# Optimization experiments

Measured on AMD Instinct MI355X. Metric: run time of the kernel, lower is better.

The kernel has to match this reference:

```python
import jax, jax.numpy as jnp
import numpy as np

IRR_IN = 4
IRR_OUT = 4
N_SCALAR = 64
E = 1_000_000
DIM = IRR_IN * IRR_OUT * 2  # 32
HID = 2 * DIM               # 64

# ir_1: swap-pair gather index [1,0,3,2,5,4,7,6]
IR_1 = np.concatenate([np.array([1, 0]) + 2 * i for i in range(IRR_IN)])
# ir_2: alternating sign [1,-1,1,-1,...]
IR_2 = np.ones(2 * IRR_IN, dtype=np.float32)
IR_2[1::2] = -1.0


def setup_inputs() -> dict:
    key = jax.random.key(0)
    ks = jax.random.split(key, 4)
    x = jax.random.normal(ks[0], (E, IRR_IN, 2), dtype=jnp.float32)
    s = jax.random.normal(ks[1], (E, N_SCALAR), dtype=jnp.float32)
    W1 = jax.random.normal(ks[2], (N_SCALAR, HID), dtype=jnp.float32) * (1.0 / np.sqrt(N_SCALAR))
    b1 = jnp.zeros((HID,), dtype=jnp.float32)
    W2 = jax.random.normal(ks[3], (HID, DIM), dtype=jnp.float32) * (1.0 / np.sqrt(HID))
    b2 = jnp.zeros((DIM,), dtype=jnp.float32)
    return {"x": x, "s": s, "W1": W1, "b1": b1, "W2": W2, "b2": b2}


def reference(x, s, W1, b1, W2, b2):
    ir1 = jnp.asarray(IR_1)
    ir2 = jnp.asarray(IR_2)
    # per-edge MLP producing raw weights: [E, irr_out, 2*irr_in]
    h = jax.nn.relu(s @ W1 + b1)
    w = (h @ W2 + b2).reshape(-1, IRR_OUT, 2 * IRR_IN)
    w_1 = w[:, :, ir1]        # pair-swapped copy
    w_2 = w * ir2             # sign-alternated copy
    # stack -> [E, 2, irr_out, 2*irr_in]; permute -> [E, 2*irr_in, irr_out, 2]
    wm = jnp.stack((w_2, w_1), axis=1).transpose(0, 3, 2, 1)
    wm = wm.reshape(-1, 2 * IRR_IN, 2 * IRR_OUT)  # [E, 2*irr_in, 2*irr_out]
    xf = x.reshape(-1, 2 * IRR_IN)                # [E, 2*irr_in]
    out = jnp.einsum('ei,eio->eo', xf, wm)        # tiny per-edge matvec
    return out.reshape(-1, IRR_OUT, 2)
```

## Files before the change

### kernel.cpp

```cpp
#include <hip/hip_runtime.h>
#include <hip/hip_bf16.h>

typedef __bf16 bf16x8 __attribute__((ext_vector_type(8)));
typedef float  f32x4  __attribute__((ext_vector_type(4)));

__global__ __launch_bounds__(256) void so2_fused_kernel(
    const float* __restrict__ x, const float* __restrict__ s,
    const float* __restrict__ W1, const float* __restrict__ b1v,
    const float* __restrict__ W2, const float* __restrict__ b2v,
    float* __restrict__ out, int E)
{
  __shared__ unsigned short lds_w1t[64 * 64];
  __shared__ unsigned short lds_w2t[32 * 64];
  __shared__ float lds_b1[64];
  __shared__ float lds_b2[32];
  __shared__ char lds_hw[4][8192];

  const int tid  = threadIdx.x;
  const int wid  = tid >> 6;
  const int lane = tid & 63;
  const int lrow = lane & 15;
  const int lg   = lane >> 4;

  const int web = blockIdx.x * 256 + wid * 64;
  const bool wave_active = (web < E);

  f32x4 sv[4][4];
  {
    const int base_e = wave_active ? web : 0;
    #pragma unroll
    for (int mt = 0; mt < 4; ++mt) {
      int er = base_e + mt * 16 + lrow;
      er = er < E ? er : E - 1;
      const float* sp = s + (size_t)er * 64 + lg * 8;
      sv[mt][0] = *(const f32x4*)(sp);
      sv[mt][1] = *(const f32x4*)(sp + 4);
      sv[mt][2] = *(const f32x4*)(sp + 32);
      sv[mt][3] = *(const f32x4*)(sp + 36);
    }
  }

  #pragma unroll
  for (int it = 0; it < 16; ++it) {
    int i = it * 256 + tid;
    int k = i >> 6, j = i & 63;
    int byte = (j << 7) + (k << 1);
    byte ^= (j & 7) << 4;
    *(unsigned short*)((char*)lds_w1t + byte) =
        __builtin_bit_cast(unsigned short, (__bf16)W1[i]);
  }
  #pragma unroll
  for (int it = 0; it < 8; ++it) {
    int i = it * 256 + tid;
    int k = i >> 5, d = i & 31;
    int byte = (d << 7) + (k << 1);
    byte ^= (d & 7) << 4;
    *(unsigned short*)((char*)lds_w2t + byte) =
        __builtin_bit_cast(unsigned short, (__bf16)W2[i]);
  }
  if (tid < 64) lds_b1[tid] = b1v[tid];
  if (tid >= 64 && tid < 96) lds_b2[tid - 64] = b2v[tid - 64];
  __syncthreads();
  if (!wave_active) return;

  char* hbuf = lds_hw[wid];

  bf16x8 af[4][2];
  #pragma unroll
  for (int mt = 0; mt < 4; ++mt) {
    #pragma unroll
    for (int h = 0; h < 2; ++h) {
      #pragma unroll
      for (int i = 0; i < 4; ++i) {
        af[mt][h][i]     = (__bf16)sv[mt][h * 2][i];
        af[mt][h][i + 4] = (__bf16)sv[mt][h * 2 + 1][i];
      }
    }
  }

  #pragma unroll
  for (int nt = 0; nt < 4; ++nt) {
    const int j = nt * 16 + lrow;
    bf16x8 bfr[2];
    #pragma unroll
    for (int h = 0; h < 2; ++h) {
      int byte = (j << 7) + ((h * 32 + lg * 8) << 1);
      byte ^= (j & 7) << 4;
      bfr[h] = *(const bf16x8*)((const char*)lds_w1t + byte);
    }
    const float bj = lds_b1[j];
    #pragma unroll
    for (int mt = 0; mt < 4; ++mt) {
      f32x4 acc = {0.f, 0.f, 0.f, 0.f};
      acc = __builtin_amdgcn_mfma_f32_16x16x32_bf16(af[mt][0], bfr[0], acc, 0, 0, 0);
      acc = __builtin_amdgcn_mfma_f32_16x16x32_bf16(af[mt][1], bfr[1], acc, 0, 0, 0);
      #pragma unroll
      for (int r = 0; r < 4; ++r) {
        float hv = fmaxf(acc[r] + bj, 0.f);
        int row = mt * 16 + lg * 4 + r;
        int byte = (row << 7) + (j << 1);
        byte ^= (row & 7) << 4;
        *(unsigned short*)(hbuf + byte) =
            __builtin_bit_cast(unsigned short, (__bf16)hv);
      }
    }
  }

  bf16x8 a2[4][2];
  #pragma unroll
  for (int mt = 0; mt < 4; ++mt) {
    #pragma unroll
    for (int h = 0; h < 2; ++h) {
      int row = mt * 16 + lrow;
      int byte = (row << 7) + ((h * 32 + lg * 8) << 1);
      byte ^= (row & 7) << 4;
      a2[mt][h] = *(const bf16x8*)(hbuf + byte);
    }
  }
  bf16x8 b2f[2][2];
  #pragma unroll
  for (int nt = 0; nt < 2; ++nt) {
    #pragma unroll
    for (int h = 0; h < 2; ++h) {
      int d = nt * 16 + lrow;
      int byte = (d << 7) + ((h * 32 + lg * 8) << 1);
      byte ^= (d & 7) << 4;
      b2f[nt][h] = *(const bf16x8*)((const char*)lds_w2t + byte);
    }
  }
  f32x4 wacc[4][2];
  #pragma unroll
  for (int mt = 0; mt < 4; ++mt) {
    #pragma unroll
    for (int nt = 0; nt < 2; ++nt) {
      f32x4 acc = {0.f, 0.f, 0.f, 0.f};
      acc = __builtin_amdgcn_mfma_f32_16x16x32_bf16(a2[mt][0], b2f[nt][0], acc, 0, 0, 0);
      acc = __builtin_amdgcn_mfma_f32_16x16x32_bf16(a2[mt][1], b2f[nt][1], acc, 0, 0, 0);
      wacc[mt][nt] = acc;
    }
  }

  #pragma unroll
  for (int nt = 0; nt < 2; ++nt) {
    const int d = nt * 16 + lrow;
    const float bd = lds_b2[d];
    #pragma unroll
    for (int mt = 0; mt < 4; ++mt) {
      f32x4 wout;
      #pragma unroll
      for (int r = 0; r < 4; ++r) wout[r] = wacc[mt][nt][r] + bd;
      int byte = (d << 8) + ((mt * 16 + lg * 4) << 2);
      byte ^= (d & 7) << 4;
      *(f32x4*)(hbuf + byte) = wout;
    }
  }

  const int e = web + lane;
  const float* xp = x + (size_t)(e < E ? e : E - 1) * 8;
  f32x4 x0 = *(const f32x4*)xp;
  f32x4 x1 = *(const f32x4*)(xp + 4);

  float wv32[32];
  #pragma unroll
  for (int d = 0; d < 32; ++d) {
    int byte = (d << 8) + (lane << 2);
    byte ^= (d & 7) << 4;
    wv32[d] = *(const float*)(hbuf + byte);
  }

  f32x4 o0, o1;
  #pragma unroll
  for (int o = 0; o < 4; ++o) {
    float orv = 0.f, oiv = 0.f;
    #pragma unroll
    for (int p = 0; p < 4; ++p) {
      float xr = (p < 2) ? x0[2 * p]     : x1[2 * p - 4];
      float xi = (p < 2) ? x0[2 * p + 1] : x1[2 * p - 3];
      float wr = wv32[o * 8 + 2 * p];
      float wi = wv32[o * 8 + 2 * p + 1];
      orv = fmaf(xr, wr, orv);
      orv = fmaf(-xi, wi, orv);
      oiv = fmaf(xr, wi, oiv);
      oiv = fmaf(xi, wr, oiv);
    }
    if (o < 2) { o0[2 * o] = orv; o0[2 * o + 1] = oiv; }
    else       { o1[2 * o - 4] = orv; o1[2 * o - 3] = oiv; }
  }
  if (e < E) {
    float* op = out + (size_t)e * 8;
    *(f32x4*)op       = o0;
    *(f32x4*)(op + 4) = o1;
  }
}

extern "C" void kernel_launch(void* const* d_in, const int* in_sizes, int n_in,
                              void* d_out, int out_size, void* d_ws, size_t ws_size,
                              hipStream_t stream) {
  const float* x  = (const float*)d_in[0];
  const float* s  = (const float*)d_in[1];
  const float* W1 = (const float*)d_in[2];
  const float* b1 = (const float*)d_in[3];
  const float* W2 = (const float*)d_in[4];
  const float* b2 = (const float*)d_in[5];
  float* out = (float*)d_out;
  const int E = in_sizes[0] / 8;
  const int blocks = (E + 255) / 256;
  so2_fused_kernel<<<blocks, 256, 0, stream>>>(x, s, W1, b1, W2, b2, out, E);
}
```

Before: 66.41 us.

## Transpose MFMA operands, fold biases into accumulators, and do the matvec in registers

Swaps the MFMA operand order so outputs come out edge-major. Biases now load straight into the accumulator init, so the bias LDS arrays go away. The final complex matvec runs directly on the MFMA accumulator fragments with a cross-lane shuffle, instead of staging the 32 weights per edge through LDS. It also vectorizes the W1/W2 global loads and the hidden-activation LDS stores, and prefetches x early; the cost is more scattered 8-byte output stores.

```diff
diff --git a/kernel.cpp b/kernel.cpp
--- a/kernel.cpp
+++ b/kernel.cpp
@@ -2,7 +2,9 @@
 #include <hip/hip_bf16.h>
 
 typedef __bf16 bf16x8 __attribute__((ext_vector_type(8)));
+typedef __bf16 bf16x4 __attribute__((ext_vector_type(4)));
 typedef float  f32x4  __attribute__((ext_vector_type(4)));
+typedef float  f32x2  __attribute__((ext_vector_type(2)));
 
 __global__ __launch_bounds__(256) void so2_fused_kernel(
     const float* __restrict__ x, const float* __restrict__ s,
@@ -12,9 +14,7 @@
 {
   __shared__ unsigned short lds_w1t[64 * 64];
   __shared__ unsigned short lds_w2t[32 * 64];
-  __shared__ float lds_b1[64];
-  __shared__ float lds_b2[32];
-  __shared__ char lds_hw[4][8192];
+  __shared__ char lds_h[4][8192];
 
   const int tid  = threadIdx.x;
   const int wid  = tid >> 6;
@@ -24,172 +24,153 @@
 
   const int web = blockIdx.x * 256 + wid * 64;
   const bool wave_active = (web < E);
+  const int base_e = wave_active ? web : 0;
 
   f32x4 sv[4][4];
-  {
-    const int base_e = wave_active ? web : 0;
+  #pragma unroll
+  for (int et = 0; et < 4; ++et) {
+    int er = base_e + et * 16 + lrow; er = er < E ? er : E - 1;
+    const float* sp = s + (size_t)er * 64 + lg * 8;
+    sv[et][0] = *(const f32x4*)(sp);
+    sv[et][1] = *(const f32x4*)(sp + 4);
+    sv[et][2] = *(const f32x4*)(sp + 32);
+    sv[et][3] = *(const f32x4*)(sp + 36);
+  }
+  f32x4 xv[4];
+  #pragma unroll
+  for (int et = 0; et < 4; ++et) {
+    int er = base_e + et * 16 + lrow; er = er < E ? er : E - 1;
+    xv[et] = *(const f32x4*)(x + (size_t)er * 8 + (lg & 1) * 4);
+  }
+  f32x4 bias1[4], bias2[2];
+  #pragma unroll
+  for (int jt = 0; jt < 4; ++jt) bias1[jt] = *(const f32x4*)(b1v + jt * 16 + lg * 4);
+  #pragma unroll
+  for (int dt = 0; dt < 2; ++dt) bias2[dt] = *(const f32x4*)(b2v + dt * 16 + lg * 4);
+
+  #pragma unroll
+  for (int it = 0; it < 4; ++it) {
+    int i = (it * 256 + tid) * 4;
+    f32x4 v = *(const f32x4*)(W1 + i);
+    int k = i >> 6, j = i & 63;
     #pragma unroll
-    for (int mt = 0; mt < 4; ++mt) {
-      int er = base_e + mt * 16 + lrow;
-      er = er < E ? er : E - 1;
-      const float* sp = s + (size_t)er * 64 + lg * 8;
-      sv[mt][0] = *(const f32x4*)(sp);
-      sv[mt][1] = *(const f32x4*)(sp + 4);
-      sv[mt][2] = *(const f32x4*)(sp + 32);
-      sv[mt][3] = *(const f32x4*)(sp + 36);
+    for (int q = 0; q < 4; ++q) {
+      int byte = ((j + q) << 7) + (k << 1);
+      byte ^= ((j + q) & 7) << 4;
+      *(unsigned short*)((char*)lds_w1t + byte) =
+          __builtin_bit_cast(unsigned short, (__bf16)v[q]);
+    }
+  }
+  #pragma unroll
+  for (int it = 0; it < 2; ++it) {
+    int i = (it * 256 + tid) * 4;
+    f32x4 v = *(const f32x4*)(W2 + i);
+    int k = i >> 5, d = i & 31;
+    #pragma unroll
+    for (int q = 0; q < 4; ++q) {
+      int byte = ((d + q) << 7) + (k << 1);
+      byte ^= ((d + q) & 7) << 4;
+      *(unsigned short*)((char*)lds_w2t + byte) =
+          __builtin_bit_cast(unsigned short, (__bf16)v[q]);
+    }
+  }
+
+  bf16x8 sf[4][2];
+  #pragma unroll
+  for (int et = 0; et < 4; ++et) {
+    #pragma unroll
+    for (int c = 0; c < 2; ++c) {
+      #pragma unroll
+      for (int i = 0; i < 4; ++i) {
+        sf[et][c][i]     = (__bf16)sv[et][c * 2][i];
+        sf[et][c][i + 4] = (__bf16)sv[et][c * 2 + 1][i];
+      }
+    }
+  }
+
+  __syncthreads();
+  if (!wave_active) return;
+
+  char* hbuf = lds_h[wid];
+
+  #pragma unroll
+  for (int jt = 0; jt < 4; ++jt) {
+    bf16x8 wf[2];
+    #pragma unroll
+    for (int c = 0; c < 2; ++c) {
+      int j = jt * 16 + lrow;
+      int byte = (j << 7) + ((c * 32 + lg * 8) << 1);
+      byte ^= (j & 7) << 4;
+      wf[c] = *(const bf16x8*)((const char*)lds_w1t + byte);
+    }
+    #pragma unroll
+    for (int et = 0; et < 4; ++et) {
+      f32x4 acc = bias1[jt];
+      acc = __builtin_amdgcn_mfma_f32_16x16x32_bf16(wf[0], sf[et][0], acc, 0, 0, 0);
+      acc = __builtin_amdgcn_mfma_f32_16x16x32_bf16(wf[1], sf[et][1], acc, 0, 0, 0);
+      bf16x4 hv;
+      #pragma unroll
+      for (int r = 0; r < 4; ++r) hv[r] = (__bf16)fmaxf(acc[r], 0.f);
+      int byte = ((et * 16 + lrow) << 7) + ((jt * 16 + lg * 4) << 1);
+      byte ^= (lrow & 7) << 4;
+      *(bf16x4*)(hbuf + byte) = hv;
+    }
+  }
+
+  asm volatile("s_waitcnt lgkmcnt(0)" ::: "memory");
+  __builtin_amdgcn_sched_barrier(0);
+
+  bf16x8 w2f[2][2];
+  #pragma unroll
+  for (int dt = 0; dt < 2; ++dt) {
+    #pragma unroll
+    for (int c = 0; c < 2; ++c) {
+      int d = dt * 16 + lrow;
+      int byte = (d << 7) + ((c * 32 + lg * 8) << 1);
+      byte ^= (d & 7) << 4;
+      w2f[dt][c] = *(const bf16x8*)((const char*)lds_w2t + byte);
+    }
+  }
+  f32x4 wacc[4][2];
+  #pragma unroll
+  for (int et = 0; et < 4; ++et) {
+    bf16x8 hf[2];
+    #pragma unroll
+    for (int c = 0; c < 2; ++c) {
+      int byte = ((et * 16 + lrow) << 7) + ((c * 32 + lg * 8) << 1);
+      byte ^= (lrow & 7) << 4;
+      hf[c] = *(const bf16x8*)(hbuf + byte);
+    }
+    #pragma unroll
+    for (int dt = 0; dt < 2; ++dt) {
+      f32x4 acc = bias2[dt];
+      acc = __builtin_amdgcn_mfma_f32_16x16x32_bf16(w2f[dt][0], hf[0], acc, 0, 0, 0);
+      acc = __builtin_amdgcn_mfma_f32_16x16x32_bf16(w2f[dt][1], hf[1], acc, 0, 0, 0);
+      wacc[et][dt] = acc;
     }
   }
 
   #pragma unroll
-  for (int it = 0; it < 16; ++it) {
-    int i = it * 256 + tid;
-    int k = i >> 6, j = i & 63;
-    int byte = (j << 7) + (k << 1);
-    byte ^= (j & 7) << 4;
-    *(unsigned short*)((char*)lds_w1t + byte) =
-        __builtin_bit_cast(unsigned short, (__bf16)W1[i]);
-  }
-  #pragma unroll
-  for (int it = 0; it < 8; ++it) {
-    int i = it * 256 + tid;
-    int k = i >> 5, d = i & 31;
-    int byte = (d << 7) + (k << 1);
-    byte ^= (d & 7) << 4;
-    *(unsigned short*)((char*)lds_w2t + byte) =
-        __builtin_bit_cast(unsigned short, (__bf16)W2[i]);
-  }
-  if (tid < 64) lds_b1[tid] = b1v[tid];
-  if (tid >= 64 && tid < 96) lds_b2[tid - 64] = b2v[tid - 64];
-  __syncthreads();
-  if (!wave_active) return;
-
-  char* hbuf = lds_hw[wid];
-
-  bf16x8 af[4][2];
-  #pragma unroll
-  for (int mt = 0; mt < 4; ++mt) {
+  for (int et = 0; et < 4; ++et) {
+    f32x4 xe = xv[et];
+    float qr[2], qi[2];
     #pragma unroll
-    for (int h = 0; h < 2; ++h) {
-      #pragma unroll
-      for (int i = 0; i < 4; ++i) {
-        af[mt][h][i]     = (__bf16)sv[mt][h * 2][i];
-        af[mt][h][i + 4] = (__bf16)sv[mt][h * 2 + 1][i];
-      }
+    for (int dt = 0; dt < 2; ++dt) {
+      f32x4 a = wacc[et][dt];
+      float pr = xe[0] * a[0] - xe[1] * a[1] + xe[2] * a[2] - xe[3] * a[3];
+      float pi = xe[0] * a[1] + xe[1] * a[0] + xe[2] * a[3] + xe[3] * a[2];
+      qr[dt] = pr + __shfl_xor(pr, 16, 64);
+      qi[dt] = pi + __shfl_xor(pi, 16, 64);
     }
-  }
-
-  #pragma unroll
-  for (int nt = 0; nt < 4; ++nt) {
-    const int j = nt * 16 + lrow;
-    bf16x8 bfr[2];
-    #pragma unroll
-    for (int h = 0; h < 2; ++h) {
-      int byte = (j << 7) + ((h * 32 + lg * 8) << 1);
-      byte ^= (j & 7) << 4;
-      bfr[h] = *(const bf16x8*)((const char*)lds_w1t + byte);
+    const int sel = lg & 1;
+    const int o = (lg >> 1) + 2 * sel;
+    const float vr = sel ? qr[1] : qr[0];
+    const float vi = sel ? qi[1] : qi[0];
+    const int e = web + et * 16 + lrow;
+    if (e < E) {
+      f32x2 v2 = {vr, vi};
+      *(f32x2*)(out + (size_t)e * 8 + o * 2) = v2;
     }
-    const float bj = lds_b1[j];
-    #pragma unroll
-    for (int mt = 0; mt < 4; ++mt) {
-      f32x4 acc = {0.f, 0.f, 0.f, 0.f};
-      acc = __builtin_amdgcn_mfma_f32_16x16x32_bf16(af[mt][0], bfr[0], acc, 0, 0, 0);
-      acc = __builtin_amdgcn_mfma_f32_16x16x32_bf16(af[mt][1], bfr[1], acc, 0, 0, 0);
-      #pragma unroll
-      for (int r = 0; r < 4; ++r) {
-        float hv = fmaxf(acc[r] + bj, 0.f);
-        int row = mt * 16 + lg * 4 + r;
-        int byte = (row << 7) + (j << 1);
-        byte ^= (row & 7) << 4;
-        *(unsigned short*)(hbuf + byte) =
-            __builtin_bit_cast(unsigned short, (__bf16)hv);
-      }
-    }
-  }
-
-  bf16x8 a2[4][2];
-  #pragma unroll
-  for (int mt = 0; mt < 4; ++mt) {
-    #pragma unroll
-    for (int h = 0; h < 2; ++h) {
-      int row = mt * 16 + lrow;
-      int byte = (row << 7) + ((h * 32 + lg * 8) << 1);
-      byte ^= (row & 7) << 4;
-      a2[mt][h] = *(const bf16x8*)(hbuf + byte);
-    }
-  }
-  bf16x8 b2f[2][2];
-  #pragma unroll
-  for (int nt = 0; nt < 2; ++nt) {
-    #pragma unroll
-    for (int h = 0; h < 2; ++h) {
-      int d = nt * 16 + lrow;
-      int byte = (d << 7) + ((h * 32 + lg * 8) << 1);
-      byte ^= (d & 7) << 4;
-      b2f[nt][h] = *(const bf16x8*)((const char*)lds_w2t + byte);
-    }
-  }
-  f32x4 wacc[4][2];
-  #pragma unroll
-  for (int mt = 0; mt < 4; ++mt) {
-    #pragma unroll
-    for (int nt = 0; nt < 2; ++nt) {
-      f32x4 acc = {0.f, 0.f, 0.f, 0.f};
-      acc = __builtin_amdgcn_mfma_f32_16x16x32_bf16(a2[mt][0], b2f[nt][0], acc, 0, 0, 0);
-      acc = __builtin_amdgcn_mfma_f32_16x16x32_bf16(a2[mt][1], b2f[nt][1], acc, 0, 0, 0);
-      wacc[mt][nt] = acc;
-    }
-  }
-
-  #pragma unroll
-  for (int nt = 0; nt < 2; ++nt) {
-    const int d = nt * 16 + lrow;
-    const float bd = lds_b2[d];
-    #pragma unroll
-    for (int mt = 0; mt < 4; ++mt) {
-      f32x4 wout;
-      #pragma unroll
-      for (int r = 0; r < 4; ++r) wout[r] = wacc[mt][nt][r] + bd;
-      int byte = (d << 8) + ((mt * 16 + lg * 4) << 2);
-      byte ^= (d & 7) << 4;
-      *(f32x4*)(hbuf + byte) = wout;
-    }
-  }
-
-  const int e = web + lane;
-  const float* xp = x + (size_t)(e < E ? e : E - 1) * 8;
-  f32x4 x0 = *(const f32x4*)xp;
-  f32x4 x1 = *(const f32x4*)(xp + 4);
-
-  float wv32[32];
-  #pragma unroll
-  for (int d = 0; d < 32; ++d) {
-    int byte = (d << 8) + (lane << 2);
-    byte ^= (d & 7) << 4;
-    wv32[d] = *(const float*)(hbuf + byte);
-  }
-
-  f32x4 o0, o1;
-  #pragma unroll
-  for (int o = 0; o < 4; ++o) {
-    float orv = 0.f, oiv = 0.f;
-    #pragma unroll
-    for (int p = 0; p < 4; ++p) {
-      float xr = (p < 2) ? x0[2 * p]     : x1[2 * p - 4];
-      float xi = (p < 2) ? x0[2 * p + 1] : x1[2 * p - 3];
-      float wr = wv32[o * 8 + 2 * p];
-      float wi = wv32[o * 8 + 2 * p + 1];
-      orv = fmaf(xr, wr, orv);
-      orv = fmaf(-xi, wi, orv);
-      oiv = fmaf(xr, wi, oiv);
-      oiv = fmaf(xi, wr, oiv);
-    }
-    if (o < 2) { o0[2 * o] = orv; o0[2 * o + 1] = oiv; }
-    else       { o1[2 * o - 4] = orv; o1[2 * o - 3] = oiv; }
-  }
-  if (e < E) {
-    float* op = out + (size_t)e * 8;
-    *(f32x4*)op       = o0;
-    *(f32x4*)(op + 4) = o1;
   }
 }
 
```

Result: slower. 68.29 us (+2.8%).
